# Kernel optimization log

Hardware: AMD Instinct MI355X
Metric: run time of the kernel (lower is better)

Reference implementation:

```python
import jax, jax.numpy as jnp
import numpy as np

B, L, D, H = 2, 2048, 1024, 16
DK = D // H
DFF = 4 * D
EPS = 1e-5  # torch LayerNorm default


def setup_inputs() -> dict:
    key = jax.random.key(0)
    ks = jax.random.split(key, 12)
    w = lambda k, shp: (jax.random.normal(k, shp, jnp.float32) * 0.02)
    return {
        "x": jax.random.normal(ks[0], (B, L, D), jnp.float32),
        "y": jax.random.normal(ks[1], (B, L, D), jnp.float32),
        "Wq": w(ks[2], (D, D)), "bq": jnp.zeros((D,), jnp.float32),
        "Wk": w(ks[3], (D, D)), "bk": jnp.zeros((D,), jnp.float32),
        "Wv": w(ks[4], (D, D)), "bv": jnp.zeros((D,), jnp.float32),
        "Wo": w(ks[5], (D, D)), "bo": jnp.zeros((D,), jnp.float32),
        "W1": w(ks[6], (D, DFF)), "b1": jnp.zeros((DFF,), jnp.float32),
        "W2": w(ks[7], (DFF, D)), "b2": jnp.zeros((D,), jnp.float32),
        "ln1_w": jnp.ones((L, D), jnp.float32), "ln1_b": jnp.zeros((L, D), jnp.float32),
        "ln2_w": jnp.ones((L, D), jnp.float32), "ln2_b": jnp.zeros((L, D), jnp.float32),
    }


def _layernorm2d(t, w, b):
    # nn.LayerNorm(normalized_shape=[L, D]): normalize jointly over last two dims
    mu = jnp.mean(t, axis=(-2, -1), keepdims=True)
    var = jnp.mean((t - mu) ** 2, axis=(-2, -1), keepdims=True)
    return (t - mu) * jax.lax.rsqrt(var + EPS) * w + b


def _attention(q_in, kv_in, Wq, bq, Wk, bk, Wv, bv, Wo, bo):
    split = lambda t: t.reshape(B, L, H, DK).transpose(0, 2, 1, 3)  # [B,H,L,DK]
    q = split(q_in @ Wq + bq)
    k = split(kv_in @ Wk + bk)
    v = split(kv_in @ Wv + bv)
    scores = jnp.einsum("bhqd,bhkd->bhqk", q, k) / (DK ** 0.5)
    # NOTE: original applies torch.tril to SCORES (zeroes upper triangle,
    # NOT -inf), so future positions still contribute exp(0)=1 in softmax.
    scores = jnp.tril(scores)
    p_attn = jax.nn.softmax(scores, axis=-1)
    out = jnp.einsum("bhqk,bhkd->bhqd", p_attn, v)
    out = out.transpose(0, 2, 1, 3).reshape(B, L, D)
    return out @ Wo + bo


def reference(x, y, Wq, bq, Wk, bk, Wv, bv, Wo, bo, W1, b1, W2, b2,
              ln1_w, ln1_b, ln2_w, ln2_b):
    # sublayer 0: pre-norm y, attention(query=x, key=value=norm(y)), residual
    y1 = y + _attention(x, _layernorm2d(y, ln1_w, ln1_b),
                        Wq, bq, Wk, bk, Wv, bv, Wo, bo)
    # sublayer 1: pre-norm, FFN (dropout inactive in eval), residual
    h = jax.nn.relu(_layernorm2d(y1, ln2_w, ln2_b) @ W1 + b1)
    return y1 + h @ W2 + b2
```

## Files before the change

kernel.cpp:

```cpp
#include <hip/hip_runtime.h>
#include <math.h>

#define B 2
#define L 2048
#define D 1024
#define H 16
#define DK 64
#define DFF 4096
#define EPS 1e-5f

typedef short short8 __attribute__((ext_vector_type(8)));
typedef short short4v __attribute__((ext_vector_type(4)));
typedef float float4v __attribute__((ext_vector_type(4)));
typedef unsigned int u32;

__device__ inline short f2bf(float f) {
    unsigned u = __builtin_bit_cast(unsigned, f);
    u += 0x7fffu + ((u >> 16) & 1u);
    return (short)(u >> 16);
}

__device__ inline float bf2f(short s) {
    unsigned u = ((unsigned)(unsigned short)s) << 16;
    return __builtin_bit_cast(float, u);
}

#define GLOAD_LDS16(gp, lp)                                                  \
    __builtin_amdgcn_global_load_lds(                                        \
        (const __attribute__((address_space(1))) u32*)(const void*)(gp),     \
        (__attribute__((address_space(3))) u32*)(void*)(lp), 16, 0, 0)

__device__ inline void xcd_remap(int& bx, int& by) {
    const int nbx = gridDim.x, nby = gridDim.y;
    const int orig = blockIdx.x + nbx * blockIdx.y;
    const int k = orig & 7, j = orig >> 3;
    const int nyc = nby >> 3;
    bx = j % nbx;
    by = k * nyc + j / nbx;
}


__global__ __launch_bounds__(256) void red_partial(const float* __restrict__ X,
                                                   float* __restrict__ part) {
    int b = blockIdx.y;
    const float4* p = (const float4*)(X + (size_t)b * L * D);
    float s = 0.f, ss = 0.f;
    for (int idx = blockIdx.x * 256 + threadIdx.x; idx < L * D / 4; idx += 256 * 256) {
        float4 v = p[idx];
        s += v.x + v.y + v.z + v.w;
        ss += v.x * v.x + v.y * v.y + v.z * v.z + v.w * v.w;
    }
    __shared__ float sh0[256], sh1[256];
    sh0[threadIdx.x] = s; sh1[threadIdx.x] = ss;
    __syncthreads();
    for (int o = 128; o; o >>= 1) {
        if (threadIdx.x < o) {
            sh0[threadIdx.x] += sh0[threadIdx.x + o];
            sh1[threadIdx.x] += sh1[threadIdx.x + o];
        }
        __syncthreads();
    }
    if (threadIdx.x == 0) {
        part[(b * 256 + blockIdx.x) * 2 + 0] = sh0[0];
        part[(b * 256 + blockIdx.x) * 2 + 1] = sh1[0];
    }
}

__global__ __launch_bounds__(256) void red_final(const float* __restrict__ part,
                                                 float* __restrict__ stats) {
    int b = blockIdx.x;
    float s = part[(b * 256 + threadIdx.x) * 2 + 0];
    float ss = part[(b * 256 + threadIdx.x) * 2 + 1];
    __shared__ float sh0[256], sh1[256];
    sh0[threadIdx.x] = s; sh1[threadIdx.x] = ss;
    __syncthreads();
    for (int o = 128; o; o >>= 1) {
        if (threadIdx.x < o) {
            sh0[threadIdx.x] += sh0[threadIdx.x + o];
            sh1[threadIdx.x] += sh1[threadIdx.x + o];
        }
        __syncthreads();
    }
    if (threadIdx.x == 0) {
        const float invN = 1.f / (float)(L * D);
        float mu = sh0[0] * invN;
        float var = sh1[0] * invN - mu * mu;
        stats[b * 2 + 0] = mu;
        stats[b * 2 + 1] = rsqrtf(var + EPS);
    }
}

__global__ __launch_bounds__(256) void ln_apply_bf(const float* __restrict__ X,
                                                   const float* __restrict__ W,
                                                   const float* __restrict__ Bb,
                                                   const float* __restrict__ stats,
                                                   short* __restrict__ Yn) {
    int b = blockIdx.y;
    float mu = stats[b * 2 + 0];
    float rstd = stats[b * 2 + 1];
    size_t e = (size_t)(blockIdx.x * 256 + threadIdx.x) * 4;
    const float4 xv = *(const float4*)(X + (size_t)b * L * D + e);
    const float4 wv = *(const float4*)(W + e);
    const float4 bv = *(const float4*)(Bb + e);
    short4v o;
    o[0] = f2bf((xv.x - mu) * rstd * wv.x + bv.x);
    o[1] = f2bf((xv.y - mu) * rstd * wv.y + bv.y);
    o[2] = f2bf((xv.z - mu) * rstd * wv.z + bv.z);
    o[3] = f2bf((xv.w - mu) * rstd * wv.w + bv.w);
    *(short4v*)(Yn + (size_t)b * L * D + e) = o;
}

__global__ __launch_bounds__(256) void convert_bf(const float* __restrict__ X,
                                                  short* __restrict__ Y) {
    size_t e = (size_t)(blockIdx.x * 256 + threadIdx.x) * 4;
    const float4 v = *(const float4*)(X + e);
    short4v o = {f2bf(v.x), f2bf(v.y), f2bf(v.z), f2bf(v.w)};
    *(short4v*)(Y + e) = o;
}

__global__ __launch_bounds__(256) void wt_transpose_all(
        const float* __restrict__ Wq, const float* __restrict__ Wk,
        const float* __restrict__ Wv, const float* __restrict__ Wo,
        const float* __restrict__ W1, const float* __restrict__ W2,
        short* __restrict__ WqT, short* __restrict__ WkvT,
        short* __restrict__ WoT, short* __restrict__ W1T,
        short* __restrict__ W2T) {
    const int id = blockIdx.x;
    const float* W; short* WT; int K, N, rel;
    if (id < 1024)      { W = Wq; WT = WqT;                    K = 1024; N = 1024; rel = id; }
    else if (id < 2048) { W = Wk; WT = WkvT;                   K = 1024; N = 1024; rel = id - 1024; }
    else if (id < 3072) { W = Wv; WT = WkvT + (size_t)D * D;   K = 1024; N = 1024; rel = id - 2048; }
    else if (id < 4096) { W = Wo; WT = WoT;                    K = 1024; N = 1024; rel = id - 3072; }
    else if (id < 8192) { W = W1; WT = W1T;                    K = 1024; N = 4096; rel = id - 4096; }
    else                { W = W2; WT = W2T;                    K = 4096; N = 1024; rel = id - 8192; }
    const int lb = (N == 4096) ? 7 : 5;
    const int bx = rel & ((1 << lb) - 1), by = rel >> lb;

    __shared__ short tile[32][33];
    const int t = threadIdx.x;
    const int tx = t & 31, ty = t >> 5;
    const int k0 = by * 32, n0 = bx * 32;
#pragma unroll
    for (int i = 0; i < 4; ++i) {
        const int k = ty + i * 8;
        tile[k][tx] = f2bf(W[(size_t)(k0 + k) * N + n0 + tx]);
    }
    __syncthreads();
#pragma unroll
    for (int i = 0; i < 4; ++i) {
        const int n = ty + i * 8;
        WT[(size_t)(n0 + n) * K + k0 + tx] = tile[tx][n];
    }
}


__device__ __forceinline__ void cv128_body(const short* __restrict__ A,
                                           const short* __restrict__ BT,
                                           const float* __restrict__ bias,
                                           const float* __restrict__ Res,
                                           void* __restrict__ Cout,
                                           int N, int Kloop, int lda, int flags,
                                           int m0, int n0,
                                           short* __restrict__ AsB,
                                           short* __restrict__ BsB) {
    const int t = threadIdx.x;
    const int wave = t >> 6, lane = t & 63;
    const int m16 = lane & 15, q4 = lane >> 4;
    const int wm = (wave >> 1) * 64, wn = (wave & 1) * 64;
    const int xorm = m16 & 7;
    const int BUFE = 128 * 64;

    float4v acc[4][4];
#pragma unroll
    for (int i = 0; i < 4; ++i)
#pragma unroll
        for (int j = 0; j < 4; ++j) acc[i][j] = (float4v){0.f, 0.f, 0.f, 0.f};

    auto stage = [&](int buf, int k0) {
        short* AsBuf = AsB + buf * BUFE;
        short* BsBuf = BsB + buf * BUFE;
#pragma unroll
        for (int p = 0; p < 4; ++p) {
            const int s = p * 256 + t;
            const int row = s >> 3;
            const int col = ((s & 7) ^ (row & 7)) * 8;
            GLOAD_LDS16(A + (size_t)(m0 + row) * lda + k0 + col,
                        AsBuf + (p * 256 + wave * 64) * 8);
        }
#pragma unroll
        for (int p = 0; p < 4; ++p) {
            const int s = p * 256 + t;
            const int row = s >> 3;
            const int col = ((s & 7) ^ (row & 7)) * 8;
            GLOAD_LDS16(BT + (size_t)(n0 + row) * lda + k0 + col,
                        BsBuf + (p * 256 + wave * 64) * 8);
        }
    };

    auto compute = [&](int buf) {
        const short* AsBuf = AsB + buf * BUFE;
        const short* BsBuf = BsB + buf * BUFE;
#pragma unroll
        for (int kk = 0; kk < 2; ++kk) {
            const int slot = ((kk * 4 + q4) ^ xorm) * 8;
            short8 af[4], bf[4];
#pragma unroll
            for (int mi = 0; mi < 4; ++mi)
                af[mi] = *(const short8*)&AsBuf[(wm + mi * 16 + m16) * 64 + slot];
#pragma unroll
            for (int ni = 0; ni < 4; ++ni)
                bf[ni] = *(const short8*)&BsBuf[(wn + ni * 16 + m16) * 64 + slot];
#pragma unroll
            for (int mi = 0; mi < 4; ++mi)
#pragma unroll
                for (int ni = 0; ni < 4; ++ni)
                    acc[mi][ni] = __builtin_amdgcn_mfma_f32_16x16x32_bf16(
                        af[mi], bf[ni], acc[mi][ni], 0, 0, 0);
        }
    };

    const int nt = Kloop >> 6;
    stage(0, 0);
    for (int ti = 0; ti < nt; ++ti) {
        const int cur = ti & 1;
        if (ti + 1 < nt) {
            stage(cur ^ 1, (ti + 1) << 6);
            asm volatile("s_waitcnt vmcnt(8)" ::: "memory");
        } else {
            asm volatile("s_waitcnt vmcnt(0)" ::: "memory");
        }
        __builtin_amdgcn_s_barrier();
        __builtin_amdgcn_sched_barrier(0);
        compute(cur);
        __builtin_amdgcn_s_barrier();
    }

#pragma unroll
    for (int mi = 0; mi < 4; ++mi)
#pragma unroll
        for (int ni = 0; ni < 4; ++ni) {
            const int col = n0 + wn + ni * 16 + m16;
            const float bb = bias ? bias[col] : 0.f;
#pragma unroll
            for (int r = 0; r < 4; ++r) {
                const int row = m0 + wm + mi * 16 + q4 * 4 + r;
                float v = acc[mi][ni][r] + bb;
                if (Res) v += Res[(size_t)row * N + col];
                if (flags & 1) v = fmaxf(v, 0.f);
                if (flags & 2)
                    ((short*)Cout)[(size_t)row * N + col] = f2bf(v);
                else
                    ((float*)Cout)[(size_t)row * N + col] = v;
            }
        }
}

__global__ __launch_bounds__(256) void gemm_qkv(const short* __restrict__ xb,
                                                const short* __restrict__ WqT,
                                                const float* __restrict__ bq,
                                                short* __restrict__ qb,
                                                const short* __restrict__ ynb,
                                                const short* __restrict__ WkvT,
                                                const float* __restrict__ bkv,
                                                short* __restrict__ kvb) {
    __shared__ short As[2][128 * 64];
    __shared__ short Bs[2][128 * 64];
    const int id = blockIdx.x;
    const int k = id & 7, j = id >> 3;
    const int lin = k * 96 + j;
    if (lin < 256) {
        const int bx = lin & 7, by = lin >> 3;
        cv128_body(xb, WqT, bq, nullptr, qb, 1024, 1024, 1024, 2,
                   by * 128, bx * 128, &As[0][0], &Bs[0][0]);
    } else {
        const int l2 = lin - 256;
        const int bx = l2 & 15, by = l2 >> 4;
        cv128_body(ynb, WkvT, bkv, nullptr, kvb, 2048, 1024, 1024, 2,
                   by * 128, bx * 128, &As[0][0], &Bs[0][0]);
    }
}

__global__ __launch_bounds__(256) void gemm_cv128_sk(const short* __restrict__ A,
                                                     const short* __restrict__ BT,
                                                     float* __restrict__ part,
                                                     int M, int N, int K) {
    __shared__ short As[2][128 * 64];
    __shared__ short Bs[2][128 * 64];
    const int id = blockIdx.x;
    const int k = id & 7, j = id >> 3;
    const int lin = k * 64 + j;
    const int ks = lin >> 8;
    const int rem = lin & 255;
    const int by = rem & 31, bx = (rem >> 5) & 7;
    const int Kc = K >> 1;
    cv128_body(A + ks * Kc, BT + ks * Kc, nullptr, nullptr,
               part + (size_t)ks * M * N, N, Kc, K, 0,
               by * 128, bx * 128, &As[0][0], &Bs[0][0]);
}

__global__ __launch_bounds__(256) void sk_reduce(const float* __restrict__ part,
                                                 const float* __restrict__ bias,
                                                 const float* __restrict__ Res,
                                                 float* __restrict__ out,
                                                 int MN, int N) {
    const size_t e = (size_t)(blockIdx.x * 256 + threadIdx.x) * 4;
    const float4 p0 = *(const float4*)(part + e);
    const float4 p1 = *(const float4*)(part + (size_t)MN + e);
    const float4 rv = *(const float4*)(Res + e);
    const float4 bv = *(const float4*)(bias + (e & (size_t)(N - 1)));
    float4 o;
    o.x = p0.x + p1.x + rv.x + bv.x;
    o.y = p0.y + p1.y + rv.y + bv.y;
    o.z = p0.z + p1.z + rv.z + bv.z;
    o.w = p0.w + p1.w + rv.w + bv.w;
    *(float4*)(out + e) = o;
}

__global__ __launch_bounds__(512) void gemm_cv256(const short* __restrict__ A,
                                                  const short* __restrict__ BT,
                                                  const float* __restrict__ bias,
                                                  const float* __restrict__ Res,
                                                  void* __restrict__ Cout,
                                                  int M, int N, int K, int flags) {
    __shared__ short As[2][256 * 64];
    __shared__ short Bs[2][256 * 64];
    const int t = threadIdx.x;
    const int wave = t >> 6, lane = t & 63;
    const int m16 = lane & 15, q4 = lane >> 4;
    int bx, by;
    xcd_remap(bx, by);
    const int m0 = by * 256, n0 = bx * 256;
    const int wm = (wave >> 2) * 128, wn = (wave & 3) * 64;
    const int xorm = m16 & 7;

    float4v acc[8][4];
#pragma unroll
    for (int i = 0; i < 8; ++i)
#pragma unroll
        for (int j = 0; j < 4; ++j) acc[i][j] = (float4v){0.f, 0.f, 0.f, 0.f};

    auto stage = [&](int buf, int k0) {
#pragma unroll
        for (int p = 0; p < 4; ++p) {
            const int s = p * 512 + t;
            const int row = s >> 3;
            const int col = ((s & 7) ^ (row & 7)) * 8;
            short* lds = &As[buf][(p * 512 + wave * 64) * 8];
            GLOAD_LDS16(A + (size_t)(m0 + row) * K + k0 + col, lds);
        }
#pragma unroll
        for (int p = 0; p < 4; ++p) {
            const int s = p * 512 + t;
            const int row = s >> 3;
            const int col = ((s & 7) ^ (row & 7)) * 8;
            short* lds = &Bs[buf][(p * 512 + wave * 64) * 8];
            GLOAD_LDS16(BT + (size_t)(n0 + row) * K + k0 + col, lds);
        }
    };

    auto compute = [&](int buf) {
#pragma unroll
        for (int kk = 0; kk < 2; ++kk) {
            const int slot = ((kk * 4 + q4) ^ xorm) * 8;
            short8 af[8], bf[4];
#pragma unroll
            for (int mi = 0; mi < 8; ++mi)
                af[mi] = *(const short8*)&As[buf][(wm + mi * 16 + m16) * 64 + slot];
#pragma unroll
            for (int ni = 0; ni < 4; ++ni)
                bf[ni] = *(const short8*)&Bs[buf][(wn + ni * 16 + m16) * 64 + slot];
#pragma unroll
            for (int mi = 0; mi < 8; ++mi)
#pragma unroll
                for (int ni = 0; ni < 4; ++ni)
                    acc[mi][ni] = __builtin_amdgcn_mfma_f32_16x16x32_bf16(
                        af[mi], bf[ni], acc[mi][ni], 0, 0, 0);
        }
    };

    const int nt = K >> 6;
    stage(0, 0);
    for (int ti = 0; ti < nt; ++ti) {
        const int cur = ti & 1;
        if (ti + 1 < nt) {
            stage(cur ^ 1, (ti + 1) << 6);
            asm volatile("s_waitcnt vmcnt(8)" ::: "memory");
        } else {
            asm volatile("s_waitcnt vmcnt(0)" ::: "memory");
        }
        __builtin_amdgcn_s_barrier();
        __builtin_amdgcn_sched_barrier(0);
        compute(cur);
        __builtin_amdgcn_s_barrier();
    }

#pragma unroll
    for (int mi = 0; mi < 8; ++mi)
#pragma unroll
        for (int ni = 0; ni < 4; ++ni) {
            const int col = n0 + wn + ni * 16 + m16;
            const float bb = bias[col];
#pragma unroll
            for (int r = 0; r < 4; ++r) {
                const int row = m0 + wm + mi * 16 + q4 * 4 + r;
                float v = acc[mi][ni][r] + bb;
                if (Res) v += Res[(size_t)row * N + col];
                if (flags & 1) v = fmaxf(v, 0.f);
                if (flags & 2)
                    ((short*)Cout)[(size_t)row * N + col] = f2bf(v);
                else
                    ((float*)Cout)[(size_t)row * N + col] = v;
            }
        }
}


#define ASTR 72
#define SKV (2 * D)

__global__ __launch_bounds__(256) void v_transpose(const short* __restrict__ KVg,
                                                   short* __restrict__ VT,
                                                   float* __restrict__ Vtile) {
    __shared__ short tile[64 * ASTR];
    __shared__ float sh[4][64];
    const int t = threadIdx.x;
    const int bh = blockIdx.x >> 5;
    const int jt = blockIdx.x & 31;
    const int b = bh >> 4, h = bh & (H - 1);
    const size_t baseV = (size_t)b * L * SKV + (size_t)h * DK + D;
    const int j0 = jt * 64;
    const int sj = t >> 3, sd8 = (t & 7) * 8, sm = t & 7;
#pragma unroll
    for (int rep = 0; rep < 2; ++rep) {
        const int j = rep * 32 + sj;
        const short8 vv = *(const short8*)(KVg + baseV + (size_t)(j0 + j) * SKV + sd8);
        const int jsw = ((((j >> 3) ^ sm) << 3) | (j & 7));
#pragma unroll
        for (int i = 0; i < 8; ++i) tile[(sd8 + i) * ASTR + jsw] = vv[i];
    }
    __syncthreads();
#pragma unroll
    for (int rep = 0; rep < 2; ++rep) {
        const int s = rep * 256 + t;
        const int d = s >> 3, c = s & 7;
        const short8 vv = *(const short8*)&tile[d * ASTR + ((c ^ (d >> 3)) << 3)];
        *(short8*)(VT + ((size_t)bh * DK + d) * L + j0 + c * 8) = vv;
    }
    {
        const int d = t & 63, g = t >> 6;
        float s = 0.f;
#pragma unroll
        for (int c = 0; c < 16; ++c) s += bf2f(tile[d * ASTR + g * 16 + c]);
        sh[g][d] = s;
        __syncthreads();
        if (t < 64)
            Vtile[((size_t)bh * 32 + jt) * 64 + t] =
                sh[0][t] + sh[1][t] + sh[2][t] + sh[3][t];
    }
}

__global__ __launch_bounds__(64) void v_suffix(const float* __restrict__ Vtile,
                                               float* __restrict__ Vsuf) {
    const int bh = blockIdx.x;
    const int d = threadIdx.x;
    float s = 0.f;
    Vsuf[((size_t)bh * 33 + 32) * 64 + d] = 0.f;
    for (int kt = 31; kt >= 0; --kt) {
        s += Vtile[((size_t)bh * 32 + kt) * 64 + d];
        Vsuf[((size_t)bh * 33 + kt) * 64 + d] = s;
    }
}


__global__ __launch_bounds__(256) void attn_mfma(const short* __restrict__ Qg,
                                                 const short* __restrict__ KVg,
                                                 const short* __restrict__ VTg,
                                                 const float* __restrict__ Vsuf,
                                                 short* __restrict__ O) {
    __shared__ alignas(16) short Kb[3][64 * 64];
    __shared__ alignas(16) short Vt[3][64 * 64];
    __shared__ alignas(16) short Pb[64 * ASTR];

    const int t = threadIdx.x;
    const int wave = t >> 6;
    const int lane = t & 63;
    const int m16 = lane & 15;
    const int q4 = lane >> 4;

    const int u = blockIdx.x & 15;
    const int bh = blockIdx.x >> 4;
    const int h = bh & (H - 1);
    const int b = bh >> 4;
    const size_t baseQ = (size_t)b * L * D + (size_t)h * DK;
    const size_t baseK = (size_t)b * L * SKV + (size_t)h * DK;
    const size_t baseVT = (size_t)bh * DK * L;

    const int irow = wave * 16 + m16;
    const int ig = irow >> 3;
    const int xorm = m16 & 7;

    auto stage = [&](int buf, int kt0) {
#pragma unroll
        for (int rep = 0; rep < 2; ++rep) {
            const int s = rep * 256 + t;
            const int j = s >> 3;
            const int c = (s & 7) ^ (j & 7);
            GLOAD_LDS16(KVg + baseK + (size_t)(kt0 + j) * SKV + c * 8,
                        &Kb[buf][(rep * 256 + wave * 64) * 8]);
        }
#pragma unroll
        for (int rep = 0; rep < 2; ++rep) {
            const int s = rep * 256 + t;
            const int d = s >> 3;
            const int c = (s & 7) ^ (d & 7);
            GLOAD_LDS16(VTg + baseVT + (size_t)d * L + kt0 + c * 8,
                        &Vt[buf][(rep * 256 + wave * 64) * 8]);
        }
    };

#pragma unroll
    for (int pq = 0; pq < 2; ++pq) {
        const int qt = pq ? (31 - u) : u;
        const int q0 = qt * 64;
        const int rowA = q0 + wave * 16 + m16;

        short8 qf[2];
#pragma unroll
        for (int kc = 0; kc < 2; ++kc)
            qf[kc] = *(const short8*)(Qg + baseQ + (size_t)rowA * D + kc * 32 + q4 * 8);

        float lsum = 0.f;
        float4v acc[4];
#pragma unroll
        for (int f = 0; f < 4; ++f) acc[f] = (float4v){0.f, 0.f, 0.f, 0.f};

        stage(0, 0);
        if (qt >= 1) stage(1, 64);
        for (int kt = 0; kt <= qt; ++kt) {
            const int cur = kt % 3;
            if (kt + 2 <= qt) {
                stage((kt + 2) % 3, (kt + 2) * 64);
                asm volatile("s_waitcnt vmcnt(8)" ::: "memory");
            } else if (kt + 1 <= qt) {
                asm volatile("s_waitcnt vmcnt(4)" ::: "memory");
            } else {
                asm volatile("s_waitcnt vmcnt(0)" ::: "memory");
            }
            __builtin_amdgcn_s_barrier();
            __builtin_amdgcn_sched_barrier(0);

            const short* KbC = &Kb[cur][0];
            const short* VtC = &Vt[cur][0];
            const bool diag = (kt == qt);

            __builtin_amdgcn_s_setprio(1);
#pragma unroll
            for (int f = 0; f < 4; ++f) {
                const int krow = f * 16 + m16;
                const short8 kf0 = *(const short8*)&KbC[krow * 64 + ((q4 ^ xorm) << 3)];
                const short8 kf1 = *(const short8*)&KbC[krow * 64 + (((4 + q4) ^ xorm) << 3)];
                float4v sv = {0.f, 0.f, 0.f, 0.f};
                sv = __builtin_amdgcn_mfma_f32_16x16x32_bf16(kf0, qf[0], sv, 0, 0, 0);
                sv = __builtin_amdgcn_mfma_f32_16x16x32_bf16(kf1, qf[1], sv, 0, 0, 0);

                float pv[4];
                if (diag) {
#pragma unroll
                    for (int r = 0; r < 4; ++r) {
                        const int jl = f * 16 + q4 * 4 + r;
                        pv[r] = (jl <= irow) ? exp2f(sv[r] * 0.18033688f) : 1.0f;
                    }
                } else {
#pragma unroll
                    for (int r = 0; r < 4; ++r) pv[r] = exp2f(sv[r] * 0.18033688f);
                }
                lsum += pv[0] + pv[1] + pv[2] + pv[3];

                u32 r0, r1;
                asm("v_cvt_pk_bf16_f32 %0, %1, %2" : "=v"(r0) : "v"(pv[0]), "v"(pv[1]));
                asm("v_cvt_pk_bf16_f32 %0, %1, %2" : "=v"(r1) : "v"(pv[2]), "v"(pv[3]));
                const int jb = f * 2 + (q4 >> 1);
                u32* pdst = (u32*)&Pb[irow * ASTR + (((jb ^ ig) << 3) | ((q4 & 1) << 2))];
                pdst[0] = r0;
                pdst[1] = r1;
            }

#pragma unroll
            for (int kc = 0; kc < 2; ++kc) {
                const short8 pf = *(const short8*)&Pb[irow * ASTR + (((kc * 4 + q4) ^ ig) << 3)];
#pragma unroll
                for (int f = 0; f < 4; ++f) {
                    const int d = f * 16 + m16;
                    const short8 vf = *(const short8*)&VtC[d * 64 + (((kc * 4 + q4) ^ xorm) << 3)];
                    acc[f] = __builtin_amdgcn_mfma_f32_16x16x32_bf16(pf, vf, acc[f], 0, 0, 0);
                }
            }
            __builtin_amdgcn_s_setprio(0);
            __builtin_amdgcn_s_barrier();
        }

        float s = lsum;
        s += __shfl_xor(s, 16);
        s += __shfl_xor(s, 32);
        s += (float)(L - (qt + 1) * 64);
        const float inv = 1.0f / s;
        float invr[4];
#pragma unroll
        for (int r = 0; r < 4; ++r) invr[r] = __shfl(inv, q4 * 4 + r);

        const float* vs = Vsuf + ((size_t)bh * 33 + qt + 1) * 64;
#pragma unroll
        for (int f = 0; f < 4; ++f) {
            const float vadd = vs[f * 16 + m16];
#pragma unroll
            for (int r = 0; r < 4; ++r) {
                const int i = q0 + wave * 16 + q4 * 4 + r;
                O[baseQ + (size_t)i * D + f * 16 + m16] = f2bf((acc[f][r] + vadd) * invr[r]);
            }
        }
    }
}


extern "C" void kernel_launch(void* const* d_in, const int* in_sizes, int n_in,
                              void* d_out, int out_size, void* d_ws, size_t ws_size,
                              hipStream_t stream) {
    const float* x    = (const float*)d_in[0];
    const float* y    = (const float*)d_in[1];
    const float* Wq   = (const float*)d_in[2];
    const float* bq   = (const float*)d_in[3];
    const float* Wk   = (const float*)d_in[4];
    const float* bk   = (const float*)d_in[5];
    const float* Wv   = (const float*)d_in[6];
    const float* bv   = (const float*)d_in[7];
    const float* Wo   = (const float*)d_in[8];
    const float* bo   = (const float*)d_in[9];
    const float* W1   = (const float*)d_in[10];
    const float* b1   = (const float*)d_in[11];
    const float* W2   = (const float*)d_in[12];
    const float* b2   = (const float*)d_in[13];
    const float* ln1w = (const float*)d_in[14];
    const float* ln1b = (const float*)d_in[15];
    const float* ln2w = (const float*)d_in[16];
    const float* ln2b = (const float*)d_in[17];
    float* out = (float*)d_out;

    const size_t F = (size_t)B * L * D;
    char* p = (char*)d_ws;
    short* xb    = (short*)p; p += F * 2;
    short* ynb   = (short*)p; p += F * 2;
    short* qb    = (short*)p; p += F * 2;
    short* kvb   = (short*)p; p += 2 * F * 2;
    short* aob   = (short*)p; p += F * 2;
    short* y1nb  = (short*)p; p += F * 2;
    short* hb    = (short*)p; p += (size_t)B * L * DFF * 2;
    float* y1    = (float*)p; p += F * 4;
    short* WqT   = (short*)p; p += (size_t)D * D * 2;
    short* WkvT  = (short*)p; p += (size_t)D * 2 * D * 2;
    short* WoT   = (short*)p; p += (size_t)D * D * 2;
    short* W1T   = (short*)p; p += (size_t)D * DFF * 2;
    short* W2T   = (short*)p; p += (size_t)D * DFF * 2;
    float* biaskv= (float*)p; p += 2 * D * 4;
    float* vtile = (float*)p; p += (size_t)B * H * 32 * DK * 4;
    float* vsuf  = (float*)p; p += (size_t)B * H * 33 * DK * 4;
    float* part  = (float*)p; p += B * 256 * 2 * 4;
    float* stats = (float*)p;

    short* vtb = hb;
    float* skpartWo = (float*)hb;
    float* skpart = (float*)qb;

    const int M = B * L;

    wt_transpose_all<<<dim3(12288), 256, 0, stream>>>(Wq, Wk, Wv, Wo, W1, W2,
                                                      WqT, WkvT, WoT, W1T, W2T);
    hipMemcpyAsync(biaskv,     bk, D * sizeof(float), hipMemcpyDeviceToDevice, stream);
    hipMemcpyAsync(biaskv + D, bv, D * sizeof(float), hipMemcpyDeviceToDevice, stream);

    convert_bf<<<dim3(F / 1024), 256, 0, stream>>>(x, xb);

    red_partial<<<dim3(256, B), 256, 0, stream>>>(y, part);
    red_final<<<dim3(B), 256, 0, stream>>>(part, stats);
    ln_apply_bf<<<dim3(L * D / 1024, B), 256, 0, stream>>>(y, ln1w, ln1b, stats, ynb);

    gemm_qkv<<<dim3(768), 256, 0, stream>>>(xb, WqT, bq, qb, ynb, WkvT, biaskv, kvb);

    v_transpose<<<dim3(B * H * 32), 256, 0, stream>>>(kvb, vtb, vtile);
    v_suffix<<<dim3(B * H), 64, 0, stream>>>(vtile, vsuf);

    attn_mfma<<<dim3(B * H * 16), 256, 0, stream>>>(qb, kvb, vtb, vsuf, aob);

    gemm_cv128_sk<<<dim3(512), 256, 0, stream>>>(aob, WoT, skpartWo, M, D, D);
    sk_reduce<<<dim3(M * D / 1024), 256, 0, stream>>>(skpartWo, bo, y, y1, M * D, D);

    red_partial<<<dim3(256, B), 256, 0, stream>>>(y1, part);
    red_final<<<dim3(B), 256, 0, stream>>>(part, stats);
    ln_apply_bf<<<dim3(L * D / 1024, B), 256, 0, stream>>>(y1, ln2w, ln2b, stats, y1nb);

    gemm_cv256<<<dim3(DFF / 256, M / 256), 512, 0, stream>>>(y1nb, W1T, b1, nullptr, hb, M, DFF, D, 3);

    gemm_cv128_sk<<<dim3(512), 256, 0, stream>>>(hb, W2T, skpart, M, D, DFF);
    sk_reduce<<<dim3(M * D / 1024), 256, 0, stream>>>(skpart, b2, y1, out, M * D, D);
}
```

Measured before the change: 410.6 us.

## Fuse LN2 statistics into split-K reduce and simplify attention pipeline

The Wo split-K reduce now also produces per-row partial sums for the second layernorm, which removes a separate pass over y1. The v_suffix kernel is removed, and each attention block instead sums the later V tiles itself in the epilogue. Inside attention, the K/V staging goes from triple to double buffering, the s_setprio hints are dropped, exp2f is replaced by __expf, and the inline-asm packed bf16 conversion is replaced by software rounding. Several of these attention edits look like they undo earlier tuning and may slow the kernel.

Measured after the change: 421.7 us. 2.7% more time.

```diff
diff --git a/kernel.cpp b/kernel.cpp
--- a/kernel.cpp
+++ b/kernel.cpp
@@ -67,10 +67,14 @@
 }
 
 __global__ __launch_bounds__(256) void red_final(const float* __restrict__ part,
-                                                 float* __restrict__ stats) {
+                                                 float* __restrict__ stats,
+                                                 int npart) {
     int b = blockIdx.x;
-    float s = part[(b * 256 + threadIdx.x) * 2 + 0];
-    float ss = part[(b * 256 + threadIdx.x) * 2 + 1];
+    float s = 0.f, ss = 0.f;
+    for (int i = threadIdx.x; i < npart; i += 256) {
+        s += part[((size_t)b * npart + i) * 2 + 0];
+        ss += part[((size_t)b * npart + i) * 2 + 1];
+    }
     __shared__ float sh0[256], sh1[256];
     sh0[threadIdx.x] = s; sh1[threadIdx.x] = ss;
     __syncthreads();
@@ -316,6 +320,42 @@
     *(float4*)(out + e) = o;
 }
 
+__global__ __launch_bounds__(256) void sk_reduce_ln(const float* __restrict__ part,
+                                                    const float* __restrict__ bias,
+                                                    const float* __restrict__ Res,
+                                                    float* __restrict__ out,
+                                                    float* __restrict__ lnpart,
+                                                    int MN) {
+    const int b = blockIdx.y;
+    const size_t e = ((size_t)b * 2048 + blockIdx.x) * 1024 + threadIdx.x * 4;
+    const float4 p0 = *(const float4*)(part + e);
+    const float4 p1 = *(const float4*)(part + (size_t)MN + e);
+    const float4 rv = *(const float4*)(Res + e);
+    const float4 bv = *(const float4*)(bias + threadIdx.x * 4);
+    float4 o;
+    o.x = p0.x + p1.x + rv.x + bv.x;
+    o.y = p0.y + p1.y + rv.y + bv.y;
+    o.z = p0.z + p1.z + rv.z + bv.z;
+    o.w = p0.w + p1.w + rv.w + bv.w;
+    *(float4*)(out + e) = o;
+    float s = o.x + o.y + o.z + o.w;
+    float ss = o.x * o.x + o.y * o.y + o.z * o.z + o.w * o.w;
+    __shared__ float sh0[256], sh1[256];
+    sh0[threadIdx.x] = s; sh1[threadIdx.x] = ss;
+    __syncthreads();
+    for (int off = 128; off; off >>= 1) {
+        if (threadIdx.x < off) {
+            sh0[threadIdx.x] += sh0[threadIdx.x + off];
+            sh1[threadIdx.x] += sh1[threadIdx.x + off];
+        }
+        __syncthreads();
+    }
+    if (threadIdx.x == 0) {
+        lnpart[((size_t)b * 2048 + blockIdx.x) * 2 + 0] = sh0[0];
+        lnpart[((size_t)b * 2048 + blockIdx.x) * 2 + 1] = sh1[0];
+    }
+}
+
 __global__ __launch_bounds__(512) void gemm_cv256(const short* __restrict__ A,
                                                   const short* __restrict__ BT,
                                                   const float* __restrict__ bias,
@@ -459,26 +499,14 @@
     }
 }
 
-__global__ __launch_bounds__(64) void v_suffix(const float* __restrict__ Vtile,
-                                               float* __restrict__ Vsuf) {
-    const int bh = blockIdx.x;
-    const int d = threadIdx.x;
-    float s = 0.f;
-    Vsuf[((size_t)bh * 33 + 32) * 64 + d] = 0.f;
-    for (int kt = 31; kt >= 0; --kt) {
-        s += Vtile[((size_t)bh * 32 + kt) * 64 + d];
-        Vsuf[((size_t)bh * 33 + kt) * 64 + d] = s;
-    }
-}
-
 
 __global__ __launch_bounds__(256) void attn_mfma(const short* __restrict__ Qg,
                                                  const short* __restrict__ KVg,
                                                  const short* __restrict__ VTg,
-                                                 const float* __restrict__ Vsuf,
+                                                 const float* __restrict__ Vtile,
                                                  short* __restrict__ O) {
-    __shared__ alignas(16) short Kb[3][64 * 64];
-    __shared__ alignas(16) short Vt[3][64 * 64];
+    __shared__ alignas(16) short Kb[2][64 * 64];
+    __shared__ alignas(16) short Vt[2][64 * 64];
     __shared__ alignas(16) short Pb[64 * ASTR];
 
     const int t = threadIdx.x;
@@ -535,13 +563,10 @@
         for (int f = 0; f < 4; ++f) acc[f] = (float4v){0.f, 0.f, 0.f, 0.f};
 
         stage(0, 0);
-        if (qt >= 1) stage(1, 64);
         for (int kt = 0; kt <= qt; ++kt) {
-            const int cur = kt % 3;
-            if (kt + 2 <= qt) {
-                stage((kt + 2) % 3, (kt + 2) * 64);
-                asm volatile("s_waitcnt vmcnt(8)" ::: "memory");
-            } else if (kt + 1 <= qt) {
+            const int cur = kt & 1;
+            if (kt < qt) {
+                stage(cur ^ 1, (kt + 1) * 64);
                 asm volatile("s_waitcnt vmcnt(4)" ::: "memory");
             } else {
                 asm volatile("s_waitcnt vmcnt(0)" ::: "memory");
@@ -553,7 +578,6 @@
             const short* VtC = &Vt[cur][0];
             const bool diag = (kt == qt);
 
-            __builtin_amdgcn_s_setprio(1);
 #pragma unroll
             for (int f = 0; f < 4; ++f) {
                 const int krow = f * 16 + m16;
@@ -568,21 +592,19 @@
 #pragma unroll
                     for (int r = 0; r < 4; ++r) {
                         const int jl = f * 16 + q4 * 4 + r;
-                        pv[r] = (jl <= irow) ? exp2f(sv[r] * 0.18033688f) : 1.0f;
+                        pv[r] = (jl <= irow) ? __expf(sv[r] * 0.125f) : 1.0f;
                     }
                 } else {
 #pragma unroll
-                    for (int r = 0; r < 4; ++r) pv[r] = exp2f(sv[r] * 0.18033688f);
+                    for (int r = 0; r < 4; ++r) pv[r] = __expf(sv[r] * 0.125f);
                 }
                 lsum += pv[0] + pv[1] + pv[2] + pv[3];
 
-                u32 r0, r1;
-                asm("v_cvt_pk_bf16_f32 %0, %1, %2" : "=v"(r0) : "v"(pv[0]), "v"(pv[1]));
-                asm("v_cvt_pk_bf16_f32 %0, %1, %2" : "=v"(r1) : "v"(pv[2]), "v"(pv[3]));
+                short4v s4;
+                s4[0] = f2bf(pv[0]); s4[1] = f2bf(pv[1]);
+                s4[2] = f2bf(pv[2]); s4[3] = f2bf(pv[3]);
                 const int jb = f * 2 + (q4 >> 1);
-                u32* pdst = (u32*)&Pb[irow * ASTR + (((jb ^ ig) << 3) | ((q4 & 1) << 2))];
-                pdst[0] = r0;
-                pdst[1] = r1;
+                *(short4v*)&Pb[irow * ASTR + (((jb ^ ig) << 3) | ((q4 & 1) << 2))] = s4;
             }
 
 #pragma unroll
@@ -595,7 +617,6 @@
                     acc[f] = __builtin_amdgcn_mfma_f32_16x16x32_bf16(pf, vf, acc[f], 0, 0, 0);
                 }
             }
-            __builtin_amdgcn_s_setprio(0);
             __builtin_amdgcn_s_barrier();
         }
 
@@ -608,14 +629,16 @@
 #pragma unroll
         for (int r = 0; r < 4; ++r) invr[r] = __shfl(inv, q4 * 4 + r);
 
-        const float* vs = Vsuf + ((size_t)bh * 33 + qt + 1) * 64;
+        const float* vt = Vtile + (size_t)bh * 32 * 64;
 #pragma unroll
         for (int f = 0; f < 4; ++f) {
-            const float vadd = vs[f * 16 + m16];
+            const int d = f * 16 + m16;
+            float vadd = 0.f;
+            for (int kt2 = qt + 1; kt2 < 32; ++kt2) vadd += vt[kt2 * 64 + d];
 #pragma unroll
             for (int r = 0; r < 4; ++r) {
                 const int i = q0 + wave * 16 + q4 * 4 + r;
-                O[baseQ + (size_t)i * D + f * 16 + m16] = f2bf((acc[f][r] + vadd) * invr[r]);
+                O[baseQ + (size_t)i * D + d] = f2bf((acc[f][r] + vadd) * invr[r]);
             }
         }
     }
@@ -662,8 +685,7 @@
     short* W2T   = (short*)p; p += (size_t)D * DFF * 2;
     float* biaskv= (float*)p; p += 2 * D * 4;
     float* vtile = (float*)p; p += (size_t)B * H * 32 * DK * 4;
-    float* vsuf  = (float*)p; p += (size_t)B * H * 33 * DK * 4;
-    float* part  = (float*)p; p += B * 256 * 2 * 4;
+    float* part  = (float*)p; p += (size_t)B * 2048 * 2 * 4;
     float* stats = (float*)p;
 
     short* vtb = hb;
@@ -680,21 +702,18 @@
     convert_bf<<<dim3(F / 1024), 256, 0, stream>>>(x, xb);
 
     red_partial<<<dim3(256, B), 256, 0, stream>>>(y, part);
-    red_final<<<dim3(B), 256, 0, stream>>>(part, stats);
+    red_final<<<dim3(B), 256, 0, stream>>>(part, stats, 256);
     ln_apply_bf<<<dim3(L * D / 1024, B), 256, 0, stream>>>(y, ln1w, ln1b, stats, ynb);
 
     gemm_qkv<<<dim3(768), 256, 0, stream>>>(xb, WqT, bq, qb, ynb, WkvT, biaskv, kvb);
 
     v_transpose<<<dim3(B * H * 32), 256, 0, stream>>>(kvb, vtb, vtile);
-    v_suffix<<<dim3(B * H), 64, 0, stream>>>(vtile, vsuf);
-
-    attn_mfma<<<dim3(B * H * 16), 256, 0, stream>>>(qb, kvb, vtb, vsuf, aob);
+
+    attn_mfma<<<dim3(B * H * 16), 256, 0, stream>>>(qb, kvb, vtb, vtile, aob);
 
     gemm_cv128_sk<<<dim3(512), 256, 0, stream>>>(aob, WoT, skpartWo, M, D, D);
-    sk_reduce<<<dim3(M * D / 1024), 256, 0, stream>>>(skpartWo, bo, y, y1, M * D, D);
-
-    red_partial<<<dim3(256, B), 256, 0, stream>>>(y1, part);
-    red_final<<<dim3(B), 256, 0, stream>>>(part, stats);
+    sk_reduce_ln<<<dim3(2048, B), 256, 0, stream>>>(skpartWo, bo, y, y1, part, M * D);
+    red_final<<<dim3(B), 256, 0, stream>>>(part, stats, 2048);
     ln_apply_bf<<<dim3(L * D / 1024, B), 256, 0, stream>>>(y1, ln2w, ln2b, stats, y1nb);
 
     gemm_cv256<<<dim3(DFF / 256, M / 256), 512, 0, stream>>>(y1nb, W1T, b1, nullptr, hb, M, DFF, D, 3);
```
